# Optimization experiments

Measured on AMD Instinct MI355X. Metric: run time of the kernel, lower is better.

## Reference

```python
import jax, jax.numpy as jnp
import numpy as np

NSIDE = 256
F = 12 * NSIDE * NSIDE  # HEALPix facet count = 786432
B, N = 64, 200000


def setup_inputs() -> dict:
    key = jax.random.key(0)
    k1, k2, k3, k4 = jax.random.split(key, 4)
    raw = jax.random.randint(k1, (B, F), 0, F, dtype=jnp.int64)
    facets_corr = jnp.where(raw % 5 == 0, jnp.int64(-1), raw)
    img0_pooled_idx = jax.random.randint(k2, (B, N), 0, F, dtype=jnp.int64)
    img1_pooled_idx = jax.random.randint(k3, (B, N), 0, F, dtype=jnp.int64)
    keypointScores1 = jax.random.normal(k4, (B, N), dtype=jnp.float32)
    return {
        "facets_corr": facets_corr,
        "img0_pooled_idx": img0_pooled_idx,
        "img1_pooled_idx": img1_pooled_idx,
        "keypointScores1": keypointScores1,
    }


def _pair(corr, idx0, idx1, scores):
    # find_facet_correspondence, vectorized:
    # img0_new_corr[i] = corr[idx0[i]]  (img1 facet id or -1)
    img0_new_corr = corr[idx0]  # [N]
    # inverse lookup: pos[f] = position of facet f in img1_pooled_idx (-1 if absent)
    pos = jnp.full((F,), -1, dtype=jnp.int32)
    pos = pos.at[idx1].set(jnp.arange(N, dtype=jnp.int32))
    gt_matches0 = jnp.where(img0_new_corr >= 0,
                            pos[jnp.clip(img0_new_corr, 0, F - 1)],
                            jnp.int32(-1))  # [N]
    # img2_corr: target[gt_matches0[i]] = i where gt_matches0[i] != -1
    valid = gt_matches0 >= 0
    scatter_idx = jnp.where(valid, gt_matches0, N)  # N -> dropped
    gt_matches1 = jnp.full((N,), -1.0, dtype=jnp.float32)
    gt_matches1 = gt_matches1.at[scatter_idx].set(
        jnp.arange(N, dtype=jnp.float32), mode="drop")
    # scores masked to keypoints that found a correspondence (COG weighting path)
    scores_masked = jnp.where(valid, scores, 0.0)
    return jnp.stack([gt_matches0.astype(jnp.float32), gt_matches1, scores_masked], 0)


def reference(facets_corr, img0_pooled_idx, img1_pooled_idx, keypointScores1):
    # output: [B, 3, N] = (gt_matches0, gt_matches1, masked scores) per image pair
    return jax.vmap(_pair)(facets_corr, img0_pooled_idx, img1_pooled_idx, keypointScores1)
```

## Files before the change

### kernel.cpp

```cpp
#include <hip/hip_runtime.h>

#define FCOUNT 786432
#define SEGBITS 13
#define SEG 8192
#define NSEG 96
#define JBITS 18
#define JMASK ((1 << JBITS) - 1)
#define ITEMS 16
#define BLK 256
#define CHUNKSZ (BLK * ITEMS)
#define ITEMS_B 4
#define CHUNKB (BLK * ITEMS_B)
#define JPT 16
#define CAPA 2400
#define CAPB 2048
#define EPT_A 10
#define EPT_B 8
#define PSTRIDE_A (NSEG * CAPA)
#define PSTRIDE_B (NSEG * CAPB)

typedef int   iv4 __attribute__((ext_vector_type(4)));
typedef float fv4 __attribute__((ext_vector_type(4)));

template <int NS> struct MsCtl {
    int hist[NS], lstart[NS], gbase[NS], cursor[NS], wsum[BLK / 64];
    int total;
};

template <int NS>
__device__ __forceinline__ void ms_zero(MsCtl<NS>& C, int tid) {
    if (tid < NS) { C.hist[tid] = 0; C.cursor[tid] = 0; }
}

template <int NS>
__device__ __forceinline__ void ms_scan_alloc(MsCtl<NS>& C, int* __restrict__ cntRow,
                                              int tid) {
    int v = (tid < NS) ? C.hist[tid] : 0;
    int lane = tid & 63, w = tid >> 6;
    #pragma unroll
    for (int d = 1; d < 64; d <<= 1) {
        int u = __shfl_up(v, d, 64);
        if (lane >= d) v += u;
    }
    if (lane == 63) C.wsum[w] = v;
    __syncthreads();
    int add = 0;
    for (int ww = 0; ww < w; ww++) add += C.wsum[ww];
    v += add;
    if (tid < NS) {
        C.lstart[tid] = v - C.hist[tid];
        C.gbase[tid] = C.hist[tid] ? atomicAdd(&cntRow[tid], C.hist[tid]) : 0;
        if (tid == NS - 1) C.total = v;
    }
}

template <bool WLOC, int NS>
__device__ __forceinline__ void ms_copy(const MsCtl<NS>& C,
                                        const int* __restrict__ staged,
                                        const unsigned char* __restrict__ stagedSeg,
                                        int* __restrict__ bktPair, int cap,
                                        int* __restrict__ locRow, int tid) {
    int total = C.total;
    for (int i = tid; i < total; i += BLK) {
        int s = stagedSeg[i];
        int d = C.gbase[s] + (i - C.lstart[s]);
        if (d < cap) {
            int e = staged[i];
            int slot = s * cap + d;
            bktPair[slot] = e;
            if (WLOC) locRow[e & JMASK] = slot;
        }
    }
}

__device__ __forceinline__ void load_chunk(const int* __restrict__ row, int jb,
                                           int N, int tid, int (&f)[ITEMS]) {
    #pragma unroll
    for (int i4 = 0; i4 < ITEMS / 4; i4++) {
        int j0 = jb + i4 * (BLK * 4) + tid * 4;
        if (j0 + 3 < N) {
            int4 vv = *reinterpret_cast<const int4*>(row + j0);
            f[i4 * 4 + 0] = vv.x; f[i4 * 4 + 1] = vv.y;
            f[i4 * 4 + 2] = vv.z; f[i4 * 4 + 3] = vv.w;
        } else {
            #pragma unroll
            for (int s = 0; s < 4; s++)
                f[i4 * 4 + s] = (j0 + s < N) ? row[j0 + s] : -1;
        }
    }
}

__global__ __launch_bounds__(BLK) void binA_kernel(
        const int* __restrict__ idx1, int* __restrict__ cnt,
        int* __restrict__ bucket, int* __restrict__ loc,
        int N, int nchunk, int b0) {
    __shared__ MsCtl<NSEG> C;
    __shared__ int staged[CHUNKSZ];
    __shared__ unsigned char stagedSeg[CHUNKSZ];
    int id = blockIdx.x, xcd = id & 7, k = id >> 3;
    int bl = xcd + 8 * (k / nchunk), chunk = k % nchunk;
    int b = b0 + bl, tid = threadIdx.x, jb = chunk * CHUNKSZ;
    int f[ITEMS];
    load_chunk(idx1 + (size_t)b * N, jb, N, tid, f);
    ms_zero(C, tid);
    __syncthreads();
    #pragma unroll
    for (int i = 0; i < ITEMS; i++)
        if (f[i] >= 0) atomicAdd(&C.hist[f[i] >> SEGBITS], 1);
    __syncthreads();
    ms_scan_alloc(C, cnt + (size_t)bl * NSEG, tid);
    __syncthreads();
    #pragma unroll
    for (int i = 0; i < ITEMS; i++) {
        if (f[i] >= 0) {
            int j = jb + (i >> 2) * (BLK * 4) + tid * 4 + (i & 3);
            int s = f[i] >> SEGBITS;
            int r = atomicAdd(&C.cursor[s], 1);
            int pos = C.lstart[s] + r;
            staged[pos] = ((f[i] & (SEG - 1)) << JBITS) | j;
            stagedSeg[pos] = (unsigned char)s;
        }
    }
    __syncthreads();
    ms_copy<true>(C, staged, stagedSeg, bucket + (size_t)bl * PSTRIDE_A, CAPA,
                  loc + (size_t)bl * N, tid);
}

__global__ __launch_bounds__(BLK) void binBp_kernel(
        const int* __restrict__ corr, const int* __restrict__ idx0,
        int* __restrict__ cnt, int* __restrict__ bktB,
        int* __restrict__ locB, int N, int nchunk, int b0) {
    __shared__ MsCtl<NSEG> C;
    __shared__ int staged[CHUNKB];
    __shared__ unsigned char stagedSeg[CHUNKB];
    int id = blockIdx.x, xcd = id & 7, k = id >> 3;
    int bl = xcd + 8 * (k / nchunk), chunk = k % nchunk;
    int b = b0 + bl, tid = threadIdx.x, jb = chunk * CHUNKB;
    const int* row = idx0 + (size_t)b * N;
    const int* crow = corr + (size_t)b * FCOUNT;
    int* locRow = locB + (size_t)bl * N;
    int j0 = jb + tid * 4;
    int f4[4];
    if (j0 + 3 < N) {
        int4 v = *reinterpret_cast<const int4*>(row + j0);
        f4[0] = v.x; f4[1] = v.y; f4[2] = v.z; f4[3] = v.w;
    } else {
        #pragma unroll
        for (int s = 0; s < 4; s++) f4[s] = (j0 + s < N) ? row[j0 + s] : -1;
    }
    int cc[ITEMS_B];
    #pragma unroll
    for (int t = 0; t < ITEMS_B; t++)
        cc[t] = (f4[t] >= 0) ? crow[f4[t]] : -2;
    ms_zero(C, tid);
    __syncthreads();
    #pragma unroll
    for (int t = 0; t < ITEMS_B; t++) {
        if (cc[t] >= 0) atomicAdd(&C.hist[cc[t] >> SEGBITS], 1);
        else if (cc[t] == -1) locRow[j0 + t] = -1;
    }
    __syncthreads();
    ms_scan_alloc(C, cnt + (size_t)bl * NSEG, tid);
    __syncthreads();
    #pragma unroll
    for (int t = 0; t < ITEMS_B; t++) {
        if (cc[t] >= 0) {
            int seg = cc[t] >> SEGBITS;
            int r = atomicAdd(&C.cursor[seg], 1);
            int pos = C.lstart[seg] + r;
            staged[pos] = ((cc[t] & (SEG - 1)) << JBITS) | (j0 + t);
            stagedSeg[pos] = (unsigned char)seg;
        }
    }
    __syncthreads();
    ms_copy<true>(C, staged, stagedSeg, bktB + (size_t)bl * PSTRIDE_B, CAPB,
                  locRow, tid);
}

__global__ __launch_bounds__(BLK) void passC_kernel(
        const int* __restrict__ cntA, int* __restrict__ bucketA,
        const int* __restrict__ cntB, int* __restrict__ bucketB) {
    __shared__ int arr[SEG];
    int id = blockIdx.x, xcd = id & 7, k = id >> 3;
    int bl = xcd + 8 * (k / NSEG), s = k % NSEG;
    int tid = threadIdx.x;
    for (int t = tid; t < SEG; t += BLK) arr[t] = -1;
    __syncthreads();
    int nA = cntA[bl * NSEG + s]; if (nA > CAPA) nA = CAPA;
    int nB = cntB[bl * NSEG + s]; if (nB > CAPB) nB = CAPB;
    int* bA = bucketA + (size_t)bl * PSTRIDE_A + s * CAPA;
    int* bB = bucketB + (size_t)bl * PSTRIDE_B + s * CAPB;
    int eA[EPT_A], eB[EPT_B], r0[EPT_B];
    #pragma unroll
    for (int t = 0; t < EPT_A; t++) {
        int i = tid + t * BLK;
        eA[t] = 0;
        if (i < nA) {
            int e = bA[i];
            eA[t] = e;
            atomicMax(&arr[e >> JBITS], e & JMASK);
        }
    }
    __syncthreads();
    #pragma unroll
    for (int t = 0; t < EPT_B; t++) {
        int i = tid + t * BLK;
        eB[t] = 0; r0[t] = -1;
        if (i < nB) {
            int e = bB[i];
            eB[t] = e;
            r0[t] = arr[e >> JBITS];
        }
    }
    #pragma unroll
    for (int t = 0; t < EPT_A; t++) {
        int i = tid + t * BLK;
        if (i < nA && arr[eA[t] >> JBITS] == (eA[t] & JMASK))
            eA[t] |= 0x80000000;
    }
    __syncthreads();
    for (int t = tid; t < SEG; t += BLK) arr[t] = -1;
    __syncthreads();
    #pragma unroll
    for (int t = 0; t < EPT_B; t++) {
        int i = tid + t * BLK;
        if (i < nB)
            atomicMax(&arr[eB[t] >> JBITS], eB[t] & JMASK);
    }
    __syncthreads();
    #pragma unroll
    for (int t = 0; t < EPT_A; t++) {
        int i = tid + t * BLK;
        if (i < nA)
            bA[i] = (eA[t] < 0) ? arr[(eA[t] >> JBITS) & (SEG - 1)] : -1;
    }
    #pragma unroll
    for (int t = 0; t < EPT_B; t++) {
        int i = tid + t * BLK;
        if (i < nB) bB[i] = r0[t];
    }
}

__global__ __launch_bounds__(BLK) void passD_kernel(
        const int* __restrict__ locA, const int* __restrict__ locB,
        const int* __restrict__ bucketA, const int* __restrict__ bucketB,
        const float* __restrict__ scores, float* __restrict__ out,
        int N, int ndblk, int b0) {
    int id = blockIdx.x, xcd = id & 7, k = id >> 3;
    int bl = xcd + 8 * (k / ndblk), jc = k % ndblk;
    int b = b0 + bl;
    int jb = jc * (BLK * JPT);
    int tid = threadIdx.x;
    const int* lA = locA + (size_t)bl * N;
    const int* lB = locB + (size_t)bl * N;
    const int* bA = bucketA + (size_t)bl * PSTRIDE_A;
    const int* bB = bucketB + (size_t)bl * PSTRIDE_B;
    const float* sc = scores + (size_t)b * N;
    size_t ob = (size_t)b * 3 * N;
    iv4 av[JPT / 4], bv[JPT / 4];
    fv4 sv[JPT / 4];
    #pragma unroll
    for (int q = 0; q < JPT / 4; q++) {
        int j = jb + q * (BLK * 4) + tid * 4;
        if (j + 3 < N) {
            av[q] = __builtin_nontemporal_load((const iv4*)(lA + j));
            bv[q] = __builtin_nontemporal_load((const iv4*)(lB + j));
            sv[q] = __builtin_nontemporal_load((const fv4*)(sc + j));
        } else {
            #pragma unroll
            for (int e = 0; e < 4; e++) {
                int jj = j + e;
                av[q][e] = (jj < N) ? lA[jj] : 0;
                bv[q][e] = (jj < N) ? lB[jj] : -1;
                sv[q][e] = (jj < N) ? sc[jj] : 0.0f;
            }
        }
    }
    int va[JPT], vb[JPT];
    #pragma unroll
    for (int t = 0; t < JPT; t++) {
        int bi = bv[t >> 2][t & 3];
        vb[t] = bB[bi < 0 ? 0 : bi];
    }
    #pragma unroll
    for (int t = 0; t < JPT; t++)
        va[t] = bA[av[t >> 2][t & 3]];
    __builtin_amdgcn_sched_barrier(0);
    #pragma unroll
    for (int q = 0; q < JPT / 4; q++) {
        int j = jb + q * (BLK * 4) + tid * 4;
        fv4 o0, o1, o2;
        #pragma unroll
        for (int e = 0; e < 4; e++) {
            int t = q * 4 + e;
            int v = (bv[q][e] < 0) ? -1 : vb[t];
            o0[e] = (float)v;
            o1[e] = (float)va[t];
            o2[e] = (v >= 0) ? sv[q][e] : 0.0f;
        }
        if (j + 3 < N) {
            __builtin_nontemporal_store(o0, (fv4*)(out + ob + j));
            __builtin_nontemporal_store(o1, (fv4*)(out + ob + N + j));
            __builtin_nontemporal_store(o2, (fv4*)(out + ob + 2 * N + j));
        } else {
            for (int e = 0; e < 4 && j + e < N; e++) {
                out[ob + j + e] = o0[e];
                out[ob + N + j + e] = o1[e];
                out[ob + 2 * N + j + e] = o2[e];
            }
        }
    }
}

extern "C" void kernel_launch(void* const* d_in, const int* in_sizes, int n_in,
                              void* d_out, int out_size, void* d_ws, size_t ws_size,
                              hipStream_t stream) {
    const int*   corr   = (const int*)d_in[0];
    const int*   idx0   = (const int*)d_in[1];
    const int*   idx1   = (const int*)d_in[2];
    const float* scores = (const float*)d_in[3];
    float* out = (float*)d_out;

    const int B = in_sizes[0] / FCOUNT;
    const int N = in_sizes[1] / B;

    size_t cntSz  = (size_t)(NSEG + NSEG) * sizeof(int);
    size_t bASz   = (size_t)PSTRIDE_A * sizeof(int);
    size_t bBSz   = (size_t)PSTRIDE_B * sizeof(int);
    size_t locSz  = (size_t)N * sizeof(int);
    size_t perPair = cntSz + bASz + bBSz + 2 * locSz;

    int CB = (int)(ws_size / perPair);
    CB &= ~7;
    if (CB > B) CB = B;
    if (CB < 8) CB = 8;

    char* p = (char*)d_ws;
    int* cntA = (int*)p; p += (size_t)CB * NSEG * sizeof(int);
    int* cntB = (int*)p; p += (size_t)CB * NSEG * sizeof(int);
    int* bktA = (int*)p; p += bASz * CB;
    int* bktB = (int*)p; p += bBSz * CB;
    int* locA = (int*)p; p += locSz * CB;
    int* locB = (int*)p;

    int nchunkA = (N + CHUNKSZ - 1) / CHUNKSZ;
    int nchunkB = (N + CHUNKB - 1) / CHUNKB;
    int ndblk   = (N + BLK * JPT - 1) / (BLK * JPT);

    for (int b0 = 0; b0 < B; b0 += CB) {
        int nb = B - b0; if (nb > CB) nb = CB;
        hipMemsetAsync(cntA, 0, cntSz * CB, stream);
        binBp_kernel<<<nb * nchunkB, BLK, 0, stream>>>(corr, idx0, cntB, bktB,
                                                       locB, N, nchunkB, b0);
        binA_kernel<<<nb * nchunkA, BLK, 0, stream>>>(idx1, cntA, bktA, locA,
                                                      N, nchunkA, b0);
        passC_kernel<<<nb * NSEG, BLK, 0, stream>>>(cntA, bktA, cntB, bktB);
        passD_kernel<<<nb * ndblk, BLK, 0, stream>>>(locA, locB, bktA, bktB,
                                                     scores, out, N, ndblk, b0);
    }
}
```

Measured before the change: 389.8 us.

## Fuse binning kernels and stage loc writes through shared memory

```diff
diff --git a/kernel.cpp b/kernel.cpp
--- a/kernel.cpp
+++ b/kernel.cpp
@@ -6,9 +6,9 @@
 #define NSEG 96
 #define JBITS 18
 #define JMASK ((1 << JBITS) - 1)
-#define ITEMS 16
 #define BLK 256
-#define CHUNKSZ (BLK * ITEMS)
+#define ITEMS_A 8
+#define CHUNKA (BLK * ITEMS_A)
 #define ITEMS_B 4
 #define CHUNKB (BLK * ITEMS_B)
 #define JPT 16
@@ -54,12 +54,13 @@
     }
 }
 
-template <bool WLOC, int NS>
-__device__ __forceinline__ void ms_copy(const MsCtl<NS>& C,
-                                        const int* __restrict__ staged,
-                                        const unsigned char* __restrict__ stagedSeg,
-                                        int* __restrict__ bktPair, int cap,
-                                        int* __restrict__ locRow, int tid) {
+template <int NS>
+__device__ __forceinline__ void ms_copy_lds(const MsCtl<NS>& C,
+                                            const int* __restrict__ staged,
+                                            const unsigned char* __restrict__ stagedSeg,
+                                            int* __restrict__ bktPair, int cap,
+                                            int* __restrict__ locStage, int jb,
+                                            int tid) {
     int total = C.total;
     for (int i = tid; i < total; i += BLK) {
         int s = stagedSeg[i];
@@ -68,113 +69,141 @@
             int e = staged[i];
             int slot = s * cap + d;
             bktPair[slot] = e;
-            if (WLOC) locRow[e & JMASK] = slot;
-        }
-    }
-}
-
-__device__ __forceinline__ void load_chunk(const int* __restrict__ row, int jb,
-                                           int N, int tid, int (&f)[ITEMS]) {
-    #pragma unroll
-    for (int i4 = 0; i4 < ITEMS / 4; i4++) {
-        int j0 = jb + i4 * (BLK * 4) + tid * 4;
+            locStage[(e & JMASK) - jb] = slot;
+        }
+    }
+}
+
+__global__ __launch_bounds__(BLK) void bin_fused_kernel(
+        const int* __restrict__ corr, const int* __restrict__ idx0,
+        const int* __restrict__ idx1, int* __restrict__ cntA,
+        int* __restrict__ cntB, int* __restrict__ bktA, int* __restrict__ bktB,
+        int* __restrict__ locA, int* __restrict__ locB,
+        int N, int nchunkB, int nchunkA, int b0) {
+    __shared__ MsCtl<NSEG> C;
+    __shared__ int staged[CHUNKA];
+    __shared__ unsigned char stagedSeg[CHUNKA];
+    __shared__ int locStage[CHUNKA];
+    int id = blockIdx.x, xcd = id & 7, k = id >> 3;
+    int per = nchunkB + nchunkA;
+    int bl = xcd + 8 * (k / per), m = k % per;
+    int b = b0 + bl, tid = threadIdx.x;
+    bool isA; int ci;
+    if (nchunkB == 2 * nchunkA) {
+        isA = (m % 3 == 2);
+        ci = isA ? m / 3 : m - (m + 1) / 3;
+    } else {
+        isA = (m >= nchunkB);
+        ci = isA ? m - nchunkB : m;
+    }
+
+    if (isA) {
+        int jb = ci * CHUNKA;
+        const int* row = idx1 + (size_t)b * N;
+        int f[ITEMS_A];
+        #pragma unroll
+        for (int q = 0; q < ITEMS_A / 4; q++) {
+            int j0 = jb + q * (BLK * 4) + tid * 4;
+            if (j0 + 3 < N) {
+                iv4 v = __builtin_nontemporal_load((const iv4*)(row + j0));
+                f[q * 4 + 0] = v[0]; f[q * 4 + 1] = v[1];
+                f[q * 4 + 2] = v[2]; f[q * 4 + 3] = v[3];
+            } else {
+                #pragma unroll
+                for (int s = 0; s < 4; s++)
+                    f[q * 4 + s] = (j0 + s < N) ? row[j0 + s] : -1;
+            }
+        }
+        for (int t = tid; t < CHUNKA; t += BLK) locStage[t] = 0;
+        ms_zero(C, tid);
+        __syncthreads();
+        #pragma unroll
+        for (int i = 0; i < ITEMS_A; i++)
+            if (f[i] >= 0) atomicAdd(&C.hist[f[i] >> SEGBITS], 1);
+        __syncthreads();
+        ms_scan_alloc(C, cntA + (size_t)bl * NSEG, tid);
+        __syncthreads();
+        #pragma unroll
+        for (int i = 0; i < ITEMS_A; i++) {
+            if (f[i] >= 0) {
+                int j = jb + (i >> 2) * (BLK * 4) + tid * 4 + (i & 3);
+                int s = f[i] >> SEGBITS;
+                int r = atomicAdd(&C.cursor[s], 1);
+                int pos = C.lstart[s] + r;
+                staged[pos] = ((f[i] & (SEG - 1)) << JBITS) | j;
+                stagedSeg[pos] = (unsigned char)s;
+            }
+        }
+        __syncthreads();
+        ms_copy_lds(C, staged, stagedSeg, bktA + (size_t)bl * PSTRIDE_A, CAPA,
+                    locStage, jb, tid);
+        __syncthreads();
+        int* lrow = locA + (size_t)bl * N;
+        #pragma unroll
+        for (int q = 0; q < ITEMS_A / 4; q++) {
+            int j0 = jb + q * (BLK * 4) + tid * 4;
+            int o = j0 - jb;
+            if (j0 + 3 < N) {
+                iv4 v = { locStage[o], locStage[o + 1], locStage[o + 2], locStage[o + 3] };
+                __builtin_nontemporal_store(v, (iv4*)(lrow + j0));
+            } else {
+                for (int e = 0; e < 4 && j0 + e < N; e++) lrow[j0 + e] = locStage[o + e];
+            }
+        }
+    } else {
+        int jb = ci * CHUNKB;
+        const int* row = idx0 + (size_t)b * N;
+        const int* crow = corr + (size_t)b * FCOUNT;
+        int j0 = jb + tid * 4;
+        int f4[4];
         if (j0 + 3 < N) {
-            int4 vv = *reinterpret_cast<const int4*>(row + j0);
-            f[i4 * 4 + 0] = vv.x; f[i4 * 4 + 1] = vv.y;
-            f[i4 * 4 + 2] = vv.z; f[i4 * 4 + 3] = vv.w;
+            iv4 v = __builtin_nontemporal_load((const iv4*)(row + j0));
+            f4[0] = v[0]; f4[1] = v[1]; f4[2] = v[2]; f4[3] = v[3];
         } else {
             #pragma unroll
-            for (int s = 0; s < 4; s++)
-                f[i4 * 4 + s] = (j0 + s < N) ? row[j0 + s] : -1;
-        }
-    }
-}
-
-__global__ __launch_bounds__(BLK) void binA_kernel(
-        const int* __restrict__ idx1, int* __restrict__ cnt,
-        int* __restrict__ bucket, int* __restrict__ loc,
-        int N, int nchunk, int b0) {
-    __shared__ MsCtl<NSEG> C;
-    __shared__ int staged[CHUNKSZ];
-    __shared__ unsigned char stagedSeg[CHUNKSZ];
-    int id = blockIdx.x, xcd = id & 7, k = id >> 3;
-    int bl = xcd + 8 * (k / nchunk), chunk = k % nchunk;
-    int b = b0 + bl, tid = threadIdx.x, jb = chunk * CHUNKSZ;
-    int f[ITEMS];
-    load_chunk(idx1 + (size_t)b * N, jb, N, tid, f);
-    ms_zero(C, tid);
-    __syncthreads();
-    #pragma unroll
-    for (int i = 0; i < ITEMS; i++)
-        if (f[i] >= 0) atomicAdd(&C.hist[f[i] >> SEGBITS], 1);
-    __syncthreads();
-    ms_scan_alloc(C, cnt + (size_t)bl * NSEG, tid);
-    __syncthreads();
-    #pragma unroll
-    for (int i = 0; i < ITEMS; i++) {
-        if (f[i] >= 0) {
-            int j = jb + (i >> 2) * (BLK * 4) + tid * 4 + (i & 3);
-            int s = f[i] >> SEGBITS;
-            int r = atomicAdd(&C.cursor[s], 1);
-            int pos = C.lstart[s] + r;
-            staged[pos] = ((f[i] & (SEG - 1)) << JBITS) | j;
-            stagedSeg[pos] = (unsigned char)s;
-        }
-    }
-    __syncthreads();
-    ms_copy<true>(C, staged, stagedSeg, bucket + (size_t)bl * PSTRIDE_A, CAPA,
-                  loc + (size_t)bl * N, tid);
-}
-
-__global__ __launch_bounds__(BLK) void binBp_kernel(
-        const int* __restrict__ corr, const int* __restrict__ idx0,
-        int* __restrict__ cnt, int* __restrict__ bktB,
-        int* __restrict__ locB, int N, int nchunk, int b0) {
-    __shared__ MsCtl<NSEG> C;
-    __shared__ int staged[CHUNKB];
-    __shared__ unsigned char stagedSeg[CHUNKB];
-    int id = blockIdx.x, xcd = id & 7, k = id >> 3;
-    int bl = xcd + 8 * (k / nchunk), chunk = k % nchunk;
-    int b = b0 + bl, tid = threadIdx.x, jb = chunk * CHUNKB;
-    const int* row = idx0 + (size_t)b * N;
-    const int* crow = corr + (size_t)b * FCOUNT;
-    int* locRow = locB + (size_t)bl * N;
-    int j0 = jb + tid * 4;
-    int f4[4];
-    if (j0 + 3 < N) {
-        int4 v = *reinterpret_cast<const int4*>(row + j0);
-        f4[0] = v.x; f4[1] = v.y; f4[2] = v.z; f4[3] = v.w;
-    } else {
-        #pragma unroll
-        for (int s = 0; s < 4; s++) f4[s] = (j0 + s < N) ? row[j0 + s] : -1;
-    }
-    int cc[ITEMS_B];
-    #pragma unroll
-    for (int t = 0; t < ITEMS_B; t++)
-        cc[t] = (f4[t] >= 0) ? crow[f4[t]] : -2;
-    ms_zero(C, tid);
-    __syncthreads();
-    #pragma unroll
-    for (int t = 0; t < ITEMS_B; t++) {
-        if (cc[t] >= 0) atomicAdd(&C.hist[cc[t] >> SEGBITS], 1);
-        else if (cc[t] == -1) locRow[j0 + t] = -1;
-    }
-    __syncthreads();
-    ms_scan_alloc(C, cnt + (size_t)bl * NSEG, tid);
-    __syncthreads();
-    #pragma unroll
-    for (int t = 0; t < ITEMS_B; t++) {
-        if (cc[t] >= 0) {
-            int seg = cc[t] >> SEGBITS;
-            int r = atomicAdd(&C.cursor[seg], 1);
-            int pos = C.lstart[seg] + r;
-            staged[pos] = ((cc[t] & (SEG - 1)) << JBITS) | (j0 + t);
-            stagedSeg[pos] = (unsigned char)seg;
-        }
-    }
-    __syncthreads();
-    ms_copy<true>(C, staged, stagedSeg, bktB + (size_t)bl * PSTRIDE_B, CAPB,
-                  locRow, tid);
+            for (int s = 0; s < 4; s++) f4[s] = (j0 + s < N) ? row[j0 + s] : -1;
+        }
+        int cc[ITEMS_B];
+        #pragma unroll
+        for (int t = 0; t < ITEMS_B; t++) {
+            int ix = f4[t] < 0 ? 0 : f4[t];
+            cc[t] = crow[ix];
+        }
+        #pragma unroll
+        for (int t = 0; t < ITEMS_B; t++)
+            if (f4[t] < 0) cc[t] = -2;
+        for (int t = tid; t < CHUNKB; t += BLK) locStage[t] = -1;
+        ms_zero(C, tid);
+        __syncthreads();
+        #pragma unroll
+        for (int t = 0; t < ITEMS_B; t++)
+            if (cc[t] >= 0) atomicAdd(&C.hist[cc[t] >> SEGBITS], 1);
+        __syncthreads();
+        ms_scan_alloc(C, cntB + (size_t)bl * NSEG, tid);
+        __syncthreads();
+        #pragma unroll
+        for (int t = 0; t < ITEMS_B; t++) {
+            if (cc[t] >= 0) {
+                int s = cc[t] >> SEGBITS;
+                int r = atomicAdd(&C.cursor[s], 1);
+                int pos = C.lstart[s] + r;
+                staged[pos] = ((cc[t] & (SEG - 1)) << JBITS) | (j0 + t);
+                stagedSeg[pos] = (unsigned char)s;
+            }
+        }
+        __syncthreads();
+        ms_copy_lds(C, staged, stagedSeg, bktB + (size_t)bl * PSTRIDE_B, CAPB,
+                    locStage, jb, tid);
+        __syncthreads();
+        int* lrow = locB + (size_t)bl * N;
+        int o = tid * 4, jw = jb + o;
+        if (jw + 3 < N) {
+            iv4 v = { locStage[o], locStage[o + 1], locStage[o + 2], locStage[o + 3] };
+            __builtin_nontemporal_store(v, (iv4*)(lrow + jw));
+        } else {
+            for (int e = 0; e < 4 && jw + e < N; e++) lrow[jw + e] = locStage[o + e];
+        }
+    }
 }
 
 __global__ __launch_bounds__(BLK) void passC_kernel(
@@ -343,17 +372,17 @@
     int* locA = (int*)p; p += locSz * CB;
     int* locB = (int*)p;
 
-    int nchunkA = (N + CHUNKSZ - 1) / CHUNKSZ;
     int nchunkB = (N + CHUNKB - 1) / CHUNKB;
+    int nchunkA = (N + CHUNKA - 1) / CHUNKA;
+    int per     = nchunkB + nchunkA;
     int ndblk   = (N + BLK * JPT - 1) / (BLK * JPT);
 
     for (int b0 = 0; b0 < B; b0 += CB) {
         int nb = B - b0; if (nb > CB) nb = CB;
-        hipMemsetAsync(cntA, 0, cntSz * CB, stream);
-        binBp_kernel<<<nb * nchunkB, BLK, 0, stream>>>(corr, idx0, cntB, bktB,
-                                                       locB, N, nchunkB, b0);
-        binA_kernel<<<nb * nchunkA, BLK, 0, stream>>>(idx1, cntA, bktA, locA,
-                                                      N, nchunkA, b0);
+        hipMemsetAsync(cntA, 0, (size_t)2 * CB * NSEG * sizeof(int), stream);
+        bin_fused_kernel<<<nb * per, BLK, 0, stream>>>(
+            corr, idx0, idx1, cntA, cntB, bktA, bktB, locA, locB,
+            N, nchunkB, nchunkA, b0);
         passC_kernel<<<nb * NSEG, BLK, 0, stream>>>(cntA, bktA, cntB, bktB);
         passD_kernel<<<nb * ndblk, BLK, 0, stream>>>(locA, locB, bktA, bktB,
                                                      scores, out, N, ndblk, b0);
```

Result: faster. 315.2 us (-19.1%).
